# Optimization experiments

Measured on AMD Instinct MI355X. Metric: run time of the kernel, lower is better.

Reference implementation:

```python
import jax, jax.numpy as jnp
import numpy as np


def gcn_conv(x, W, b, src, dst, n_nodes):
    """PyG GCNConv: linear transform, add self-loops, symmetric deg^-1/2 norm, scatter-add, bias."""
    h = x @ W  # [N, out] transform first (out_dim <= in_dim keeps gather traffic low)
    loop = jnp.arange(n_nodes)
    s = jnp.concatenate([src, loop])  # sources incl. self-loops
    d = jnp.concatenate([dst, loop])  # targets incl. self-loops
    deg = jnp.zeros((n_nodes,), h.dtype).at[d].add(jnp.ones((), h.dtype))
    dinv = jax.lax.rsqrt(deg)  # deg >= 1 because of self-loops
    coef = (dinv[s] * dinv[d])[:, None]  # [E+N, 1]
    out = jax.ops.segment_sum(h[s] * coef, d, num_segments=n_nodes)
    return out + b


def setup_inputs() -> dict:
    key = jax.random.key(0)
    k1, k2, k3, k4 = jax.random.split(key, 4)
    N, E = 100000, 1600000
    IN, HID, OUT = 128, 64, 32
    x = jax.random.normal(k1, (N, IN), dtype=jnp.float32)
    edge_index = jax.random.randint(k2, (2, E), 0, N, dtype=jnp.int64)
    W1 = jax.random.normal(k3, (IN, HID), dtype=jnp.float32) * (1.0 / np.sqrt(IN))
    b1 = jnp.zeros((HID,), jnp.float32)
    W2 = jax.random.normal(k4, (HID, OUT), dtype=jnp.float32) * (1.0 / np.sqrt(HID))
    b2 = jnp.zeros((OUT,), jnp.float32)
    return {"x": x, "edge_index": edge_index, "W1": W1, "b1": b1, "W2": W2, "b2": b2}


def reference(x, edge_index, W1, b1, W2, b2):
    src, dst = edge_index[0], edge_index[1]
    n = x.shape[0]
    h = jax.nn.relu(gcn_conv(x, W1, b1, src, dst, n))
    return gcn_conv(h, W2, b2, src, dst, n)
```

## Files before the change

kernel.cpp:

```cpp
#include <hip/hip_runtime.h>
#include <hip/hip_bf16.h>


#define IN_DIM 128
#define HID_DIM 64
#define OUT_DIM 32
#define BSHIFT 8
#define BSIZE 256
#define BMASK 255
#define PEB 8192
#define PTHREADS 512
#define CAPSHIFT 13

typedef __attribute__((ext_vector_type(2))) float v2f;
typedef __attribute__((ext_vector_type(8))) short short8v;
typedef __attribute__((ext_vector_type(4))) float float4v;

__device__ inline unsigned pack_bf16x2(float a, float b) {
    unsigned ua = __float_as_uint(a), ub = __float_as_uint(b);
    unsigned ra = (ua + 0x7fffu + ((ua >> 16) & 1u)) >> 16;
    unsigned rb = (ub + 0x7fffu + ((ub >> 16) & 1u)) & 0xffff0000u;
    return (ra & 0xffffu) | rb;
}
__device__ inline unsigned short f2bf(float f) {
    unsigned u = __float_as_uint(f);
    return (unsigned short)((u + 0x7fffu + ((u >> 16) & 1u)) >> 16);
}
#define BF_LO(w) __uint_as_float((w) << 16)
#define BF_HI(w) __uint_as_float((w) & 0xffff0000u)

__device__ inline v2f bfpair(unsigned u) {
    v2f r;
    r.x = __uint_as_float(u << 16);
    r.y = __uint_as_float(u & 0xffff0000u);
    return r;
}

#define ACC8(q)                                         \
    do {                                                \
        acc[0] += BF_LO((q).x); acc[1] += BF_HI((q).x); \
        acc[2] += BF_LO((q).y); acc[3] += BF_HI((q).y); \
        acc[4] += BF_LO((q).z); acc[5] += BF_HI((q).z); \
        acc[6] += BF_LO((q).w); acc[7] += BF_HI((q).w); \
    } while (0)

__global__ __launch_bounds__(PTHREADS) void k_partition(const int* __restrict__ src,
                                                        const int* __restrict__ dst, int E,
                                                        int* __restrict__ bfill,
                                                        unsigned* __restrict__ packed, int B) {
    __shared__ int cnt[512];
    __shared__ int off[512];
    int t = threadIdx.x;
    if (t < 512) cnt[t] = 0;
    __syncthreads();
    int base = blockIdx.x * PEB;
    int dv[PEB / PTHREADS];
#pragma unroll
    for (int i = 0; i < PEB / PTHREADS; ++i) {
        int e = base + i * PTHREADS + t;
        dv[i] = (e < E) ? dst[e] : -1;
        if (dv[i] >= 0) atomicAdd(&cnt[dv[i] >> BSHIFT], 1);
    }
    __syncthreads();
    for (int b = t; b < B; b += PTHREADS) {
        int c = cnt[b];
        int o = c ? atomicAdd(&bfill[b], c) : 0;
        off[b] = (b << CAPSHIFT) + o;
    }
    __syncthreads();
#pragma unroll
    for (int i = 0; i < PEB / PTHREADS; ++i) {
        int e = base + i * PTHREADS + t;
        int d = dv[i];
        if (d >= 0) {
            int s = src[e];
            int slot = atomicAdd(&off[d >> BSHIFT], 1);
            packed[slot] = ((unsigned)s << BSHIFT) | (unsigned)(d & BMASK);
        }
    }
}

__global__ __launch_bounds__(512) void k_csrfill(const unsigned* __restrict__ packed,
                                                 const int* __restrict__ bfill,
                                                 int* __restrict__ colidx,
                                                 uint2* __restrict__ rowptr2,
                                                 float* __restrict__ dinv,
                                                 int N, int B) {
    __shared__ int ldeg[256];
    __shared__ int lscan[256];
    __shared__ int sexc[256];
    __shared__ int lfill[256];
    int t = threadIdx.x, bkt = blockIdx.x;
    int base = bkt << CAPSHIFT;
    int end  = base + bfill[bkt];
    if (t < 256) ldeg[t] = 0;
    __syncthreads();
    for (int e = base + t; e < end; e += 512)
        atomicAdd(&ldeg[packed[e] & BMASK], 1);
    __syncthreads();
    int v = (t < 256) ? ldeg[t] : 0;
    if (t < 256) lscan[t] = v;
    __syncthreads();
    for (int off = 1; off < 256; off <<= 1) {
        int x = (t < 256 && t >= off) ? lscan[t - off] : 0;
        __syncthreads();
        if (t < 256) lscan[t] += x;
        __syncthreads();
    }
    if (t < 256) {
        int exc = lscan[t] - v;
        sexc[t] = exc;
        lfill[t] = 0;
        int node = (bkt << BSHIFT) + t;
        if (node < N) {
            rowptr2[node] = make_uint2((unsigned)(base + exc), (unsigned)(base + exc + v));
            dinv[node] = rsqrtf((float)v + 1.0f);
        }
    }
    __syncthreads();
    for (int e = base + t; e < end; e += 512) {
        unsigned w = packed[e];
        int ld = w & BMASK;
        int pos = base + sexc[ld] + atomicAdd(&lfill[ld], 1);
        colidx[pos] = (int)(w >> BSHIFT);
    }
}

__global__ __launch_bounds__(256) void k_gemm1(const float* __restrict__ x,
                                               const float* __restrict__ W,
                                               const float* __restrict__ dinv,
                                               unsigned* __restrict__ g1b, int N) {
    __shared__ unsigned xs[16 * 66];
    int t = threadIdx.x;
    int row0 = blockIdx.x * 16;
    int w = t >> 6, lane = t & 63;
    int quad = lane >> 4, m = lane & 15;
    int ncol = w * 16 + m;

    union { unsigned u[4]; short8v s; } bf[4];
#pragma unroll
    for (int kt = 0; kt < 4; ++kt) {
#pragma unroll
        for (int jp = 0; jp < 4; ++jp) {
            int k0 = kt * 32 + quad * 8 + jp * 2;
            float f0 = W[(size_t)k0 * HID_DIM + ncol];
            float f1 = W[(size_t)(k0 + 1) * HID_DIM + ncol];
            bf[kt].u[jp] = pack_bf16x2(f0, f1);
        }
    }

#pragma unroll
    for (int i = 0; i < 2; ++i) {
        int idx = t + 256 * i;
        int r = idx >> 5, c4 = idx & 31;
        int grow = row0 + r;
        float4 f = make_float4(0.f, 0.f, 0.f, 0.f);
        if (grow < N) f = ((const float4*)x)[(size_t)grow * 32 + c4];
        xs[r * 66 + c4 * 2]     = pack_bf16x2(f.x, f.y);
        xs[r * 66 + c4 * 2 + 1] = pack_bf16x2(f.z, f.w);
    }
    __syncthreads();

    float4v acc = {0.f, 0.f, 0.f, 0.f};
#pragma unroll
    for (int kt = 0; kt < 4; ++kt) {
        union { unsigned u[4]; short8v s; } af;
        const unsigned* ap = &xs[m * 66 + kt * 16 + quad * 4];
        af.u[0] = ap[0]; af.u[1] = ap[1]; af.u[2] = ap[2]; af.u[3] = ap[3];
        acc = __builtin_amdgcn_mfma_f32_16x16x32_bf16(af.s, bf[kt].s, acc, 0, 0, 0);
    }

    unsigned short* g1s = (unsigned short*)g1b;
#pragma unroll
    for (int reg = 0; reg < 4; ++reg) {
        int r = row0 + quad * 4 + reg;
        if (r < N) {
            float dv = dinv[r];
            g1s[(size_t)r * HID_DIM + ncol] = f2bf(acc[reg] * dv);
        }
    }
}

__global__ __launch_bounds__(128) void k_agg1(const unsigned* __restrict__ g1,
                                              const uint2* __restrict__ rowptr2,
                                              const int* __restrict__ colidx,
                                              const float* __restrict__ dinv,
                                              const float* __restrict__ b1,
                                              unsigned* __restrict__ t1b, int N) {
    int t = threadIdx.x;
    int lane = t & 63;
    int q = lane >> 4, ql = lane & 15;
    int grp = ql >> 3, fp = ql & 7;
    int dd = blockIdx.x * 8 + (t >> 6) * 4 + q;
    bool live = dd < N;
    int d = live ? dd : N - 1;

    uint2 be = rowptr2[d];
    v2f a01 = {0.f, 0.f}, a23 = {0.f, 0.f}, a45 = {0.f, 0.f}, a67 = {0.f, 0.f};
#define ACC8V(qv)                                    \
    do {                                             \
        a01 += bfpair((qv).x); a23 += bfpair((qv).y);\
        a45 += bfpair((qv).z); a67 += bfpair((qv).w);\
    } while (0)
    int e = (int)be.x, end = (int)be.y;
    for (; e + 4 <= end; e += 4) {
        int s0 = colidx[e + grp];
        int s1 = colidx[e + 2 + grp];
        uint4 q0 = *(const uint4*)&g1[(size_t)s0 * 32 + fp * 4];
        uint4 q1 = *(const uint4*)&g1[(size_t)s1 * 32 + fp * 4];
        ACC8V(q0);
        ACC8V(q1);
    }
    for (; e + 2 <= end; e += 2) {
        int s = colidx[e + grp];
        uint4 qv = *(const uint4*)&g1[(size_t)s * 32 + fp * 4];
        ACC8V(qv);
    }
    if (e < end) {
        int s = colidx[e];
        uint4 qv = *(const uint4*)&g1[(size_t)s * 32 + fp * 4];
        if (grp == 0) ACC8V(qv);
    }
#undef ACC8V
    float acc[8] = {a01.x, a01.y, a23.x, a23.y, a45.x, a45.y, a67.x, a67.y};
#pragma unroll
    for (int i = 0; i < 8; ++i)
        acc[i] += __shfl_xor(acc[i], 8);

    uint4 sq = *(const uint4*)&g1[(size_t)d * 32 + fp * 4];
    ACC8(sq);
    float dv = dinv[d];
    float4 bb0 = ((const float4*)b1)[fp * 2];
    float4 bb1 = ((const float4*)b1)[fp * 2 + 1];
    float v0 = fmaxf(dv * acc[0] + bb0.x, 0.f);
    float v1 = fmaxf(dv * acc[1] + bb0.y, 0.f);
    float v2 = fmaxf(dv * acc[2] + bb0.z, 0.f);
    float v3 = fmaxf(dv * acc[3] + bb0.w, 0.f);
    float v4 = fmaxf(dv * acc[4] + bb1.x, 0.f);
    float v5 = fmaxf(dv * acc[5] + bb1.y, 0.f);
    float v6 = fmaxf(dv * acc[6] + bb1.z, 0.f);
    float v7 = fmaxf(dv * acc[7] + bb1.w, 0.f);
    if (live && grp == 0) {
        uint4 u;
        u.x = pack_bf16x2(v0, v1);
        u.y = pack_bf16x2(v2, v3);
        u.z = pack_bf16x2(v4, v5);
        u.w = pack_bf16x2(v6, v7);
        *(uint4*)&t1b[(size_t)dd * 32 + fp * 4] = u;
    }
}

__global__ __launch_bounds__(256) void k_gemm2b(const unsigned* __restrict__ t1b,
                                                const float* __restrict__ W2,
                                                const float* __restrict__ dinv,
                                                unsigned* __restrict__ g2b, int N) {
    __shared__ float t1s[64 * 68];
    __shared__ float W2s[HID_DIM * OUT_DIM];
    int t = threadIdx.x;
    int row0 = blockIdx.x * 64;

    const float4* W24 = (const float4*)W2;
    float4* W2s4 = (float4*)W2s;
    W2s4[t] = W24[t];
    W2s4[t + 256] = W24[t + 256];
#pragma unroll
    for (int i = 0; i < 8; ++i) {
        int idx = t + 256 * i;
        int r = idx >> 5, c = idx & 31;
        int grow = row0 + r;
        unsigned u = 0;
        if (grow < N) u = t1b[(size_t)grow * 32 + c];
        float2 f;
        f.x = BF_LO(u);
        f.y = BF_HI(u);
        *(float2*)&t1s[r * 68 + c * 2] = f;
    }
    __syncthreads();

    int ty = t >> 3;
    int tx = t & 7;
    float acc[2][4] = {};
#pragma unroll 4
    for (int k = 0; k < 64; k += 4) {
        float a[2][4], b[4][4];
#pragma unroll
        for (int i = 0; i < 2; ++i)
            *(float4*)a[i] = *(const float4*)&t1s[(ty * 2 + i) * 68 + k];
#pragma unroll
        for (int kk = 0; kk < 4; ++kk)
            *(float4*)b[kk] = *(const float4*)&W2s[(k + kk) * OUT_DIM + tx * 4];
#pragma unroll
        for (int i = 0; i < 2; ++i)
#pragma unroll
            for (int kk = 0; kk < 4; ++kk)
#pragma unroll
                for (int j = 0; j < 4; ++j)
                    acc[i][j] += a[i][kk] * b[kk][j];
    }
#pragma unroll
    for (int i = 0; i < 2; ++i) {
        int row = row0 + ty * 2 + i;
        if (row < N) {
            float dv = dinv[row];
            uint2 u;
            u.x = pack_bf16x2(acc[i][0] * dv, acc[i][1] * dv);
            u.y = pack_bf16x2(acc[i][2] * dv, acc[i][3] * dv);
            *(uint2*)&g2b[(size_t)row * 16 + tx * 2] = u;
        }
    }
}

__global__ __launch_bounds__(128) void k_agg2(const unsigned* __restrict__ g2,
                                              const uint2* __restrict__ rowptr2,
                                              const int* __restrict__ colidx,
                                              const float* __restrict__ dinv,
                                              const float* __restrict__ b2,
                                              float* __restrict__ out, int N) {
    int t = threadIdx.x;
    int lane = t & 63;
    int o = lane >> 3, ol = lane & 7;
    int grp = ol >> 2, fp = ol & 3;
    int dd = blockIdx.x * 16 + (t >> 6) * 8 + o;
    bool live = dd < N;
    int d = live ? dd : N - 1;

    uint2 be = rowptr2[d];
    v2f a01 = {0.f, 0.f}, a23 = {0.f, 0.f}, a45 = {0.f, 0.f}, a67 = {0.f, 0.f};
#define ACC8V(qv)                                    \
    do {                                             \
        a01 += bfpair((qv).x); a23 += bfpair((qv).y);\
        a45 += bfpair((qv).z); a67 += bfpair((qv).w);\
    } while (0)
    int e = (int)be.x, end = (int)be.y;
    for (; e + 4 <= end; e += 4) {
        int s0 = colidx[e + grp];
        int s1 = colidx[e + 2 + grp];
        uint4 q0 = *(const uint4*)&g2[(size_t)s0 * 16 + fp * 4];
        uint4 q1 = *(const uint4*)&g2[(size_t)s1 * 16 + fp * 4];
        ACC8V(q0);
        ACC8V(q1);
    }
    for (; e + 2 <= end; e += 2) {
        int s = colidx[e + grp];
        uint4 qv = *(const uint4*)&g2[(size_t)s * 16 + fp * 4];
        ACC8V(qv);
    }
    if (e < end) {
        int s = colidx[e];
        uint4 qv = *(const uint4*)&g2[(size_t)s * 16 + fp * 4];
        if (grp == 0) ACC8V(qv);
    }
#undef ACC8V
    float acc[8] = {a01.x, a01.y, a23.x, a23.y, a45.x, a45.y, a67.x, a67.y};
#pragma unroll
    for (int i = 0; i < 8; ++i)
        acc[i] += __shfl_xor(acc[i], 4);
    uint4 sq = *(const uint4*)&g2[(size_t)d * 16 + fp * 4];
    ACC8(sq);
    float dv = dinv[d];
    float4 bb0 = ((const float4*)b2)[fp * 2];
    float4 bb1 = ((const float4*)b2)[fp * 2 + 1];
    if (live && grp == 0) {
        float4 r0, r1;
        r0.x = dv * acc[0] + bb0.x; r0.y = dv * acc[1] + bb0.y;
        r0.z = dv * acc[2] + bb0.z; r0.w = dv * acc[3] + bb0.w;
        r1.x = dv * acc[4] + bb1.x; r1.y = dv * acc[5] + bb1.y;
        r1.z = dv * acc[6] + bb1.z; r1.w = dv * acc[7] + bb1.w;
        *(float4*)&out[(size_t)dd * OUT_DIM + fp * 8] = r0;
        *(float4*)&out[(size_t)dd * OUT_DIM + fp * 8 + 4] = r1;
    }
}

extern "C" void kernel_launch(void* const* d_in, const int* in_sizes, int n_in,
                              void* d_out, int out_size, void* d_ws, size_t ws_size,
                              hipStream_t stream) {
    const float* x  = (const float*)d_in[0];
    const int*   ei = (const int*)d_in[1];
    const float* W1 = (const float*)d_in[2];
    const float* b1 = (const float*)d_in[3];
    const float* W2 = (const float*)d_in[4];
    const float* b2 = (const float*)d_in[5];
    float* out = (float*)d_out;

    const int N = in_sizes[0] / IN_DIM;
    const int E = in_sizes[1] / 2;
    const int* src = ei;
    const int* dst = ei + E;

    const int B   = (N + BSIZE - 1) / BSIZE;
    const int nPB = (E + PEB - 1) / PEB;
    const size_t SLOTS = (size_t)B << CAPSHIFT;

    char* p = (char*)d_ws;
    auto alloc = [&](size_t bytes) -> void* {
        void* r = (void*)p;
        p += (bytes + 255) & ~(size_t)255;
        return r;
    };
    int*      bfill   = (int*)alloc((size_t)B * 4);
    unsigned* packed  = (unsigned*)alloc(SLOTS * 4);
    int*      colidx  = (int*)alloc(SLOTS * 4);
    uint2*    rowptr2 = (uint2*)alloc((size_t)N * 8);
    float*    dinv    = (float*)alloc((size_t)N * 4);
    unsigned* g1b     = (unsigned*)alloc((size_t)N * 32 * 4);
    unsigned* t1b     = (unsigned*)alloc((size_t)N * 32 * 4);
    unsigned* g2b     = (unsigned*)alloc((size_t)N * 16 * 4);

    hipMemsetAsync(bfill, 0, (size_t)B * 4, stream);
    k_partition<<<nPB, PTHREADS, 0, stream>>>(src, dst, E, bfill, packed, B);
    k_csrfill<<<B, 512, 0, stream>>>(packed, bfill, colidx, rowptr2, dinv, N, B);

    k_gemm1<<<(N + 15) / 16, 256, 0, stream>>>(x, W1, dinv, g1b, N);
    k_agg1<<<(N + 7) / 8, 128, 0, stream>>>(g1b, rowptr2, colidx, dinv, b1, t1b, N);
    k_gemm2b<<<(N + 63) / 64, 256, 0, stream>>>(t1b, W2, dinv, g2b, N);
    k_agg2<<<(N + 15) / 16, 128, 0, stream>>>(g2b, rowptr2, colidx, dinv, b2, out, N);
}
```

Measured before the change: 218.3 us.

## Fuse gemm1 into partition launch and fuse agg1 with MFMA gemm2

The first GEMM no longer depends on dinv, so its blocks are appended to the edge-partition launch and run concurrently with it; the source-side dinv scaling moves into the layer-1 aggregation as a per-edge gather of dinv. Layer-1 aggregation now keeps its 16-row tile of activations in shared memory and immediately runs the second GEMM with MFMA, using a split-bf16 hi/lo W2 for accuracy. This removes the t1 intermediate round trip and two kernel launches. In exchange it adds an extra dinv gather per edge and leaves half the waves idle during the small fused GEMM.

Result: faster. 207.8 us (-4.8%).

```diff
diff --git a/kernel.cpp b/kernel.cpp
--- a/kernel.cpp
+++ b/kernel.cpp
@@ -35,6 +35,10 @@
     r.y = __uint_as_float(u & 0xffff0000u);
     return r;
 }
+__device__ inline void accp(v2f& a, unsigned u, float dv) {
+    a.x += BF_LO(u) * dv;
+    a.y += BF_HI(u) * dv;
+}
 
 #define ACC8(q)                                         \
     do {                                                \
@@ -44,38 +48,89 @@
         acc[6] += BF_LO((q).w); acc[7] += BF_HI((q).w); \
     } while (0)
 
-__global__ __launch_bounds__(PTHREADS) void k_partition(const int* __restrict__ src,
-                                                        const int* __restrict__ dst, int E,
-                                                        int* __restrict__ bfill,
-                                                        unsigned* __restrict__ packed, int B) {
+__global__ __launch_bounds__(PTHREADS) void k_part_gemm1(
+        const int* __restrict__ src, const int* __restrict__ dst, int E,
+        int* __restrict__ bfill, unsigned* __restrict__ packed, int B, int nPB,
+        const float* __restrict__ x, const float* __restrict__ W,
+        unsigned* __restrict__ g1b, int N) {
     __shared__ int cnt[512];
     __shared__ int off[512];
+    __shared__ unsigned xs[32 * 66];
     int t = threadIdx.x;
-    if (t < 512) cnt[t] = 0;
-    __syncthreads();
-    int base = blockIdx.x * PEB;
-    int dv[PEB / PTHREADS];
-#pragma unroll
-    for (int i = 0; i < PEB / PTHREADS; ++i) {
-        int e = base + i * PTHREADS + t;
-        dv[i] = (e < E) ? dst[e] : -1;
-        if (dv[i] >= 0) atomicAdd(&cnt[dv[i] >> BSHIFT], 1);
-    }
-    __syncthreads();
-    for (int b = t; b < B; b += PTHREADS) {
-        int c = cnt[b];
-        int o = c ? atomicAdd(&bfill[b], c) : 0;
-        off[b] = (b << CAPSHIFT) + o;
-    }
-    __syncthreads();
-#pragma unroll
-    for (int i = 0; i < PEB / PTHREADS; ++i) {
-        int e = base + i * PTHREADS + t;
-        int d = dv[i];
-        if (d >= 0) {
-            int s = src[e];
-            int slot = atomicAdd(&off[d >> BSHIFT], 1);
-            packed[slot] = ((unsigned)s << BSHIFT) | (unsigned)(d & BMASK);
+
+    if (blockIdx.x < nPB) {
+        if (t < 512) cnt[t] = 0;
+        __syncthreads();
+        int base = blockIdx.x * PEB;
+        int dv[PEB / PTHREADS];
+#pragma unroll
+        for (int i = 0; i < PEB / PTHREADS; ++i) {
+            int e = base + i * PTHREADS + t;
+            dv[i] = (e < E) ? dst[e] : -1;
+            if (dv[i] >= 0) atomicAdd(&cnt[dv[i] >> BSHIFT], 1);
+        }
+        __syncthreads();
+        for (int b = t; b < B; b += PTHREADS) {
+            int c = cnt[b];
+            int o = c ? atomicAdd(&bfill[b], c) : 0;
+            off[b] = (b << CAPSHIFT) + o;
+        }
+        __syncthreads();
+#pragma unroll
+        for (int i = 0; i < PEB / PTHREADS; ++i) {
+            int e = base + i * PTHREADS + t;
+            int d = dv[i];
+            if (d >= 0) {
+                int s = src[e];
+                int slot = atomicAdd(&off[d >> BSHIFT], 1);
+                packed[slot] = ((unsigned)s << BSHIFT) | (unsigned)(d & BMASK);
+            }
+        }
+    } else {
+        int row0 = (blockIdx.x - nPB) * 32;
+        int w = t >> 6, lane = t & 63;
+        int rg = w >> 2, wv = w & 3;
+        int quad = lane >> 4, m = lane & 15;
+        int ncol = wv * 16 + m;
+
+        union { unsigned u[4]; short8v s; } bf[4];
+#pragma unroll
+        for (int kt = 0; kt < 4; ++kt) {
+#pragma unroll
+            for (int jp = 0; jp < 4; ++jp) {
+                int k0 = kt * 32 + quad * 8 + jp * 2;
+                float f0 = W[(size_t)k0 * HID_DIM + ncol];
+                float f1 = W[(size_t)(k0 + 1) * HID_DIM + ncol];
+                bf[kt].u[jp] = pack_bf16x2(f0, f1);
+            }
+        }
+
+#pragma unroll
+        for (int i = 0; i < 2; ++i) {
+            int idx = t + 512 * i;
+            int r = idx >> 5, c4 = idx & 31;
+            int grow = row0 + r;
+            float4 f = make_float4(0.f, 0.f, 0.f, 0.f);
+            if (grow < N) f = ((const float4*)x)[(size_t)grow * 32 + c4];
+            xs[r * 66 + c4 * 2]     = pack_bf16x2(f.x, f.y);
+            xs[r * 66 + c4 * 2 + 1] = pack_bf16x2(f.z, f.w);
+        }
+        __syncthreads();
+
+        float4v acc = {0.f, 0.f, 0.f, 0.f};
+#pragma unroll
+        for (int kt = 0; kt < 4; ++kt) {
+            union { unsigned u[4]; short8v s; } af;
+            const unsigned* ap = &xs[(rg * 16 + m) * 66 + kt * 16 + quad * 4];
+            af.u[0] = ap[0]; af.u[1] = ap[1]; af.u[2] = ap[2]; af.u[3] = ap[3];
+            acc = __builtin_amdgcn_mfma_f32_16x16x32_bf16(af.s, bf[kt].s, acc, 0, 0, 0);
+        }
+
+        unsigned short* g1s = (unsigned short*)g1b;
+#pragma unroll
+        for (int reg = 0; reg < 4; ++reg) {
+            int r = row0 + rg * 16 + quad * 4 + reg;
+            if (r < N) g1s[(size_t)r * HID_DIM + ncol] = f2bf(acc[reg]);
         }
     }
 }
@@ -126,186 +181,115 @@
     }
 }
 
-__global__ __launch_bounds__(256) void k_gemm1(const float* __restrict__ x,
-                                               const float* __restrict__ W,
-                                               const float* __restrict__ dinv,
-                                               unsigned* __restrict__ g1b, int N) {
-    __shared__ unsigned xs[16 * 66];
+__global__ __launch_bounds__(256) void k_agg1g2(const unsigned* __restrict__ g1,
+                                                const uint2* __restrict__ rowptr2,
+                                                const int* __restrict__ colidx,
+                                                const float* __restrict__ dinv,
+                                                const float* __restrict__ b1,
+                                                const float* __restrict__ W2,
+                                                unsigned short* __restrict__ g2s, int N) {
+    __shared__ unsigned t1s[16 * 33];
     int t = threadIdx.x;
-    int row0 = blockIdx.x * 16;
-    int w = t >> 6, lane = t & 63;
-    int quad = lane >> 4, m = lane & 15;
-    int ncol = w * 16 + m;
-
-    union { unsigned u[4]; short8v s; } bf[4];
-#pragma unroll
-    for (int kt = 0; kt < 4; ++kt) {
-#pragma unroll
-        for (int jp = 0; jp < 4; ++jp) {
-            int k0 = kt * 32 + quad * 8 + jp * 2;
-            float f0 = W[(size_t)k0 * HID_DIM + ncol];
-            float f1 = W[(size_t)(k0 + 1) * HID_DIM + ncol];
-            bf[kt].u[jp] = pack_bf16x2(f0, f1);
-        }
-    }
-
-#pragma unroll
-    for (int i = 0; i < 2; ++i) {
-        int idx = t + 256 * i;
-        int r = idx >> 5, c4 = idx & 31;
-        int grow = row0 + r;
-        float4 f = make_float4(0.f, 0.f, 0.f, 0.f);
-        if (grow < N) f = ((const float4*)x)[(size_t)grow * 32 + c4];
-        xs[r * 66 + c4 * 2]     = pack_bf16x2(f.x, f.y);
-        xs[r * 66 + c4 * 2 + 1] = pack_bf16x2(f.z, f.w);
-    }
-    __syncthreads();
-
-    float4v acc = {0.f, 0.f, 0.f, 0.f};
-#pragma unroll
-    for (int kt = 0; kt < 4; ++kt) {
-        union { unsigned u[4]; short8v s; } af;
-        const unsigned* ap = &xs[m * 66 + kt * 16 + quad * 4];
-        af.u[0] = ap[0]; af.u[1] = ap[1]; af.u[2] = ap[2]; af.u[3] = ap[3];
-        acc = __builtin_amdgcn_mfma_f32_16x16x32_bf16(af.s, bf[kt].s, acc, 0, 0, 0);
-    }
-
-    unsigned short* g1s = (unsigned short*)g1b;
-#pragma unroll
-    for (int reg = 0; reg < 4; ++reg) {
-        int r = row0 + quad * 4 + reg;
-        if (r < N) {
-            float dv = dinv[r];
-            g1s[(size_t)r * HID_DIM + ncol] = f2bf(acc[reg] * dv);
-        }
-    }
-}
-
-__global__ __launch_bounds__(128) void k_agg1(const unsigned* __restrict__ g1,
-                                              const uint2* __restrict__ rowptr2,
-                                              const int* __restrict__ colidx,
-                                              const float* __restrict__ dinv,
-                                              const float* __restrict__ b1,
-                                              unsigned* __restrict__ t1b, int N) {
-    int t = threadIdx.x;
-    int lane = t & 63;
+    int wave = t >> 6, lane = t & 63;
     int q = lane >> 4, ql = lane & 15;
     int grp = ql >> 3, fp = ql & 7;
-    int dd = blockIdx.x * 8 + (t >> 6) * 4 + q;
+    int nl = wave * 4 + q;
+    int dd = blockIdx.x * 16 + nl;
     bool live = dd < N;
     int d = live ? dd : N - 1;
 
     uint2 be = rowptr2[d];
     v2f a01 = {0.f, 0.f}, a23 = {0.f, 0.f}, a45 = {0.f, 0.f}, a67 = {0.f, 0.f};
-#define ACC8V(qv)                                    \
-    do {                                             \
-        a01 += bfpair((qv).x); a23 += bfpair((qv).y);\
-        a45 += bfpair((qv).z); a67 += bfpair((qv).w);\
-    } while (0)
     int e = (int)be.x, end = (int)be.y;
     for (; e + 4 <= end; e += 4) {
         int s0 = colidx[e + grp];
         int s1 = colidx[e + 2 + grp];
+        float dv0 = dinv[s0], dv1 = dinv[s1];
         uint4 q0 = *(const uint4*)&g1[(size_t)s0 * 32 + fp * 4];
         uint4 q1 = *(const uint4*)&g1[(size_t)s1 * 32 + fp * 4];
-        ACC8V(q0);
-        ACC8V(q1);
+        accp(a01, q0.x, dv0); accp(a23, q0.y, dv0);
+        accp(a45, q0.z, dv0); accp(a67, q0.w, dv0);
+        accp(a01, q1.x, dv1); accp(a23, q1.y, dv1);
+        accp(a45, q1.z, dv1); accp(a67, q1.w, dv1);
     }
     for (; e + 2 <= end; e += 2) {
         int s = colidx[e + grp];
+        float dv = dinv[s];
         uint4 qv = *(const uint4*)&g1[(size_t)s * 32 + fp * 4];
-        ACC8V(qv);
+        accp(a01, qv.x, dv); accp(a23, qv.y, dv);
+        accp(a45, qv.z, dv); accp(a67, qv.w, dv);
     }
     if (e < end) {
         int s = colidx[e];
+        float dv = dinv[s];
         uint4 qv = *(const uint4*)&g1[(size_t)s * 32 + fp * 4];
-        if (grp == 0) ACC8V(qv);
-    }
-#undef ACC8V
+        if (grp == 0) {
+            accp(a01, qv.x, dv); accp(a23, qv.y, dv);
+            accp(a45, qv.z, dv); accp(a67, qv.w, dv);
+        }
+    }
     float acc[8] = {a01.x, a01.y, a23.x, a23.y, a45.x, a45.y, a67.x, a67.y};
 #pragma unroll
     for (int i = 0; i < 8; ++i)
         acc[i] += __shfl_xor(acc[i], 8);
 
     uint4 sq = *(const uint4*)&g1[(size_t)d * 32 + fp * 4];
-    ACC8(sq);
-    float dv = dinv[d];
+    float dvd = dinv[d];
+    acc[0] += BF_LO(sq.x) * dvd; acc[1] += BF_HI(sq.x) * dvd;
+    acc[2] += BF_LO(sq.y) * dvd; acc[3] += BF_HI(sq.y) * dvd;
+    acc[4] += BF_LO(sq.z) * dvd; acc[5] += BF_HI(sq.z) * dvd;
+    acc[6] += BF_LO(sq.w) * dvd; acc[7] += BF_HI(sq.w) * dvd;
     float4 bb0 = ((const float4*)b1)[fp * 2];
     float4 bb1 = ((const float4*)b1)[fp * 2 + 1];
-    float v0 = fmaxf(dv * acc[0] + bb0.x, 0.f);
-    float v1 = fmaxf(dv * acc[1] + bb0.y, 0.f);
-    float v2 = fmaxf(dv * acc[2] + bb0.z, 0.f);
-    float v3 = fmaxf(dv * acc[3] + bb0.w, 0.f);
-    float v4 = fmaxf(dv * acc[4] + bb1.x, 0.f);
-    float v5 = fmaxf(dv * acc[5] + bb1.y, 0.f);
-    float v6 = fmaxf(dv * acc[6] + bb1.z, 0.f);
-    float v7 = fmaxf(dv * acc[7] + bb1.w, 0.f);
-    if (live && grp == 0) {
-        uint4 u;
-        u.x = pack_bf16x2(v0, v1);
-        u.y = pack_bf16x2(v2, v3);
-        u.z = pack_bf16x2(v4, v5);
-        u.w = pack_bf16x2(v6, v7);
-        *(uint4*)&t1b[(size_t)dd * 32 + fp * 4] = u;
-    }
-}
-
-__global__ __launch_bounds__(256) void k_gemm2b(const unsigned* __restrict__ t1b,
-                                                const float* __restrict__ W2,
-                                                const float* __restrict__ dinv,
-                                                unsigned* __restrict__ g2b, int N) {
-    __shared__ float t1s[64 * 68];
-    __shared__ float W2s[HID_DIM * OUT_DIM];
-    int t = threadIdx.x;
-    int row0 = blockIdx.x * 64;
-
-    const float4* W24 = (const float4*)W2;
-    float4* W2s4 = (float4*)W2s;
-    W2s4[t] = W24[t];
-    W2s4[t + 256] = W24[t + 256];
-#pragma unroll
-    for (int i = 0; i < 8; ++i) {
-        int idx = t + 256 * i;
-        int r = idx >> 5, c = idx & 31;
-        int grow = row0 + r;
-        unsigned u = 0;
-        if (grow < N) u = t1b[(size_t)grow * 32 + c];
-        float2 f;
-        f.x = BF_LO(u);
-        f.y = BF_HI(u);
-        *(float2*)&t1s[r * 68 + c * 2] = f;
+    float v0 = fmaxf(dvd * acc[0] + bb0.x, 0.f);
+    float v1 = fmaxf(dvd * acc[1] + bb0.y, 0.f);
+    float v2 = fmaxf(dvd * acc[2] + bb0.z, 0.f);
+    float v3 = fmaxf(dvd * acc[3] + bb0.w, 0.f);
+    float v4 = fmaxf(dvd * acc[4] + bb1.x, 0.f);
+    float v5 = fmaxf(dvd * acc[5] + bb1.y, 0.f);
+    float v6 = fmaxf(dvd * acc[6] + bb1.z, 0.f);
+    float v7 = fmaxf(dvd * acc[7] + bb1.w, 0.f);
+    if (grp == 0) {
+        t1s[nl * 33 + fp * 4 + 0] = pack_bf16x2(v0, v1);
+        t1s[nl * 33 + fp * 4 + 1] = pack_bf16x2(v2, v3);
+        t1s[nl * 33 + fp * 4 + 2] = pack_bf16x2(v4, v5);
+        t1s[nl * 33 + fp * 4 + 3] = pack_bf16x2(v6, v7);
     }
     __syncthreads();
 
-    int ty = t >> 3;
-    int tx = t & 7;
-    float acc[2][4] = {};
-#pragma unroll 4
-    for (int k = 0; k < 64; k += 4) {
-        float a[2][4], b[4][4];
-#pragma unroll
-        for (int i = 0; i < 2; ++i)
-            *(float4*)a[i] = *(const float4*)&t1s[(ty * 2 + i) * 68 + k];
-#pragma unroll
-        for (int kk = 0; kk < 4; ++kk)
-            *(float4*)b[kk] = *(const float4*)&W2s[(k + kk) * OUT_DIM + tx * 4];
-#pragma unroll
-        for (int i = 0; i < 2; ++i)
-#pragma unroll
-            for (int kk = 0; kk < 4; ++kk)
-#pragma unroll
-                for (int j = 0; j < 4; ++j)
-                    acc[i][j] += a[i][kk] * b[kk][j];
-    }
-#pragma unroll
-    for (int i = 0; i < 2; ++i) {
-        int row = row0 + ty * 2 + i;
-        if (row < N) {
-            float dv = dinv[row];
-            uint2 u;
-            u.x = pack_bf16x2(acc[i][0] * dv, acc[i][1] * dv);
-            u.y = pack_bf16x2(acc[i][2] * dv, acc[i][3] * dv);
-            *(uint2*)&g2b[(size_t)row * 16 + tx * 2] = u;
+    if (wave < 2) {
+        int quad = lane >> 4, n = lane & 15;
+        int col = (wave << 4) + n;
+        union { unsigned u[4]; short8v s; } af0, af1, bh0, bh1, bl0, bl1;
+#pragma unroll
+        for (int jp = 0; jp < 4; ++jp) {
+            int k0 = quad * 8 + jp * 2;
+            float f0 = W2[(size_t)k0 * OUT_DIM + col];
+            float f1 = W2[(size_t)(k0 + 1) * OUT_DIM + col];
+            float f2 = W2[(size_t)(k0 + 32) * OUT_DIM + col];
+            float f3 = W2[(size_t)(k0 + 33) * OUT_DIM + col];
+            unsigned short h0 = f2bf(f0), h1 = f2bf(f1);
+            unsigned short h2 = f2bf(f2), h3 = f2bf(f3);
+            bh0.u[jp] = (unsigned)h0 | ((unsigned)h1 << 16);
+            bh1.u[jp] = (unsigned)h2 | ((unsigned)h3 << 16);
+            float r0 = f0 - __uint_as_float((unsigned)h0 << 16);
+            float r1 = f1 - __uint_as_float((unsigned)h1 << 16);
+            float r2 = f2 - __uint_as_float((unsigned)h2 << 16);
+            float r3 = f3 - __uint_as_float((unsigned)h3 << 16);
+            bl0.u[jp] = pack_bf16x2(r0, r1);
+            bl1.u[jp] = pack_bf16x2(r2, r3);
+            af0.u[jp] = t1s[n * 33 + quad * 4 + jp];
+            af1.u[jp] = t1s[n * 33 + 16 + quad * 4 + jp];
+        }
+        float4v acc2 = {0.f, 0.f, 0.f, 0.f};
+        acc2 = __builtin_amdgcn_mfma_f32_16x16x32_bf16(af0.s, bh0.s, acc2, 0, 0, 0);
+        acc2 = __builtin_amdgcn_mfma_f32_16x16x32_bf16(af1.s, bh1.s, acc2, 0, 0, 0);
+        acc2 = __builtin_amdgcn_mfma_f32_16x16x32_bf16(af0.s, bl0.s, acc2, 0, 0, 0);
+        acc2 = __builtin_amdgcn_mfma_f32_16x16x32_bf16(af1.s, bl1.s, acc2, 0, 0, 0);
+#pragma unroll
+        for (int reg = 0; reg < 4; ++reg) {
+            int row = blockIdx.x * 16 + quad * 4 + reg;
+            if (row < N) g2s[(size_t)row * 32 + col] = f2bf(acc2[reg] * dinv[row]);
         }
     }
 }
@@ -389,6 +373,7 @@
 
     const int B   = (N + BSIZE - 1) / BSIZE;
     const int nPB = (E + PEB - 1) / PEB;
+    const int nGB = (N + 31) / 32;
     const size_t SLOTS = (size_t)B << CAPSHIFT;
 
     char* p = (char*)d_ws;
@@ -403,15 +388,13 @@
     uint2*    rowptr2 = (uint2*)alloc((size_t)N * 8);
     float*    dinv    = (float*)alloc((size_t)N * 4);
     unsigned* g1b     = (unsigned*)alloc((size_t)N * 32 * 4);
-    unsigned* t1b     = (unsigned*)alloc((size_t)N * 32 * 4);
     unsigned* g2b     = (unsigned*)alloc((size_t)N * 16 * 4);
 
     hipMemsetAsync(bfill, 0, (size_t)B * 4, stream);
-    k_partition<<<nPB, PTHREADS, 0, stream>>>(src, dst, E, bfill, packed, B);
+    k_part_gemm1<<<nPB + nGB, PTHREADS, 0, stream>>>(src, dst, E, bfill, packed, B, nPB,
+                                                     x, W1, g1b, N);
     k_csrfill<<<B, 512, 0, stream>>>(packed, bfill, colidx, rowptr2, dinv, N, B);
-
-    k_gemm1<<<(N + 15) / 16, 256, 0, stream>>>(x, W1, dinv, g1b, N);
-    k_agg1<<<(N + 7) / 8, 128, 0, stream>>>(g1b, rowptr2, colidx, dinv, b1, t1b, N);
-    k_gemm2b<<<(N + 63) / 64, 256, 0, stream>>>(t1b, W2, dinv, g2b, N);
+    k_agg1g2<<<(N + 15) / 16, 256, 0, stream>>>(g1b, rowptr2, colidx, dinv, b1, W2,
+                                                (unsigned short*)g2b, N);
     k_agg2<<<(N + 15) / 16, 128, 0, stream>>>(g2b, rowptr2, colidx, dinv, b2, out, N);
 }
```
